# Kernel tuning notes

Measured on AMD Instinct MI355X. Metric: run time of the kernel, lower is better.

Reference implementation:

```python
import jax, jax.numpy as jnp
import numpy as np

CROP_H = 14
CROP_W = 14
EXTRAPOLATION_VALUE = 0.0


def _crop_and_resize(image, boxes, box_ind, crop_h, crop_w, extrapolation_value):
    # image: [B, C, H, W], boxes: [N, 4] normalized (y1, x1, y2, x2), box_ind: [N]
    B, C, H, W = image.shape
    y1, x1, y2, x2 = boxes[:, 0], boxes[:, 1], boxes[:, 2], boxes[:, 3]

    # TF crop_and_resize coordinate mapping (crop_h, crop_w > 1 case)
    height_scale = (y2 - y1) * (H - 1) / (crop_h - 1)  # [N]
    width_scale = (x2 - x1) * (W - 1) / (crop_w - 1)   # [N]
    iy = jnp.arange(crop_h, dtype=image.dtype)
    ix = jnp.arange(crop_w, dtype=image.dtype)
    in_y = y1[:, None] * (H - 1) + iy[None, :] * height_scale[:, None]  # [N, crop_h]
    in_x = x1[:, None] * (W - 1) + ix[None, :] * width_scale[:, None]   # [N, crop_w]

    valid_y = (in_y >= 0) & (in_y <= H - 1)  # [N, crop_h]
    valid_x = (in_x >= 0) & (in_x <= W - 1)  # [N, crop_w]

    top = jnp.floor(in_y)
    left = jnp.floor(in_x)
    ly = (in_y - top)[:, :, None, None]   # [N, crop_h, 1, 1]
    lx = (in_x - left)[:, None, :, None]  # [N, 1, crop_w, 1]

    top_i = jnp.clip(top.astype(jnp.int32), 0, H - 1)          # [N, crop_h]
    bot_i = jnp.clip(top_i + 1, 0, H - 1)
    left_i = jnp.clip(left.astype(jnp.int32), 0, W - 1)        # [N, crop_w]
    right_i = jnp.clip(left_i + 1, 0, W - 1)

    b = box_ind[:, None, None]            # [N, 1, 1]
    yt = top_i[:, :, None]                # [N, crop_h, 1]
    yb = bot_i[:, :, None]
    xl = left_i[:, None, :]               # [N, 1, crop_w]
    xr = right_i[:, None, :]

    # advanced indexing -> [N, crop_h, crop_w, C]
    tl = image[b, :, yt, xl]
    tr = image[b, :, yt, xr]
    bl = image[b, :, yb, xl]
    br = image[b, :, yb, xr]

    top_v = tl + (tr - tl) * lx
    bot_v = bl + (br - bl) * lx
    val = top_v + (bot_v - top_v) * ly    # [N, crop_h, crop_w, C]

    mask = (valid_y[:, :, None] & valid_x[:, None, :])[:, :, :, None]
    val = jnp.where(mask, val, jnp.asarray(extrapolation_value, image.dtype))
    return jnp.transpose(val, (0, 3, 1, 2))  # [N, C, crop_h, crop_w]


def setup_inputs() -> dict:
    key = jax.random.key(0)
    k1, k2, k3 = jax.random.split(key, 3)
    B, C, H, W = 8, 256, 200, 200
    N = 1000
    image = jax.random.normal(k1, (B, C, H, W), dtype=jnp.float32)
    boxes = jax.random.uniform(k2, (N, 4), dtype=jnp.float32)
    box_ind = jax.random.randint(k3, (N,), 0, B, dtype=jnp.int32)
    return {"image": image, "boxes": boxes, "box_ind": box_ind}


def reference(image, boxes, box_ind):
    return _crop_and_resize(image, boxes, box_ind, CROP_H, CROP_W, EXTRAPOLATION_VALUE)
```

## Files before the change

### kernel.cpp

```cpp
#include <hip/hip_runtime.h>


#define CROP_H 14
#define CROP_W 14
#define C_DIM 256
#define H_DIM 200
#define W_DIM 200
#define PER_BOX (C_DIM * CROP_H * CROP_W)
#define BLOCK 256

__global__ __launch_bounds__(BLOCK) void crop_and_resize_kernel(
    const float* __restrict__ image,
    const float* __restrict__ boxes,
    const int*   __restrict__ box_ind,
    float*       __restrict__ out)
{
    __shared__ int   s_ti[CROP_H], s_bi[CROP_H];
    __shared__ int   s_li[CROP_W], s_ri[CROP_W];
    __shared__ float s_ly[CROP_H], s_lx[CROP_W];
    __shared__ int   s_vy[CROP_H], s_vx[CROP_W];
    __shared__ int   s_b;

    const int n = blockIdx.x;
    const int t = threadIdx.x;

    if (t == 0) s_b = box_ind[n];
    if (t < CROP_H + CROP_W) {
        const float y1 = boxes[n * 4 + 0];
        const float x1 = boxes[n * 4 + 1];
        const float y2 = boxes[n * 4 + 2];
        const float x2 = boxes[n * 4 + 3];
        if (t < CROP_H) {
            const int iy = t;
            const float hs   = (y2 - y1) * (float)(H_DIM - 1) / (float)(CROP_H - 1);
            const float in_y = y1 * (float)(H_DIM - 1) + (float)iy * hs;
            const int   vy   = (in_y >= 0.0f) && (in_y <= (float)(H_DIM - 1));
            const float top  = floorf(in_y);
            const float ly   = in_y - top;
            int ti = (int)top;
            ti = min(max(ti, 0), H_DIM - 1);
            const int bi = min(ti + 1, H_DIM - 1);
            s_ti[iy] = ti; s_bi[iy] = bi; s_ly[iy] = ly; s_vy[iy] = vy;
        } else {
            const int ix = t - CROP_H;
            const float ws   = (x2 - x1) * (float)(W_DIM - 1) / (float)(CROP_W - 1);
            const float in_x = x1 * (float)(W_DIM - 1) + (float)ix * ws;
            const int   vx   = (in_x >= 0.0f) && (in_x <= (float)(W_DIM - 1));
            const float left = floorf(in_x);
            const float lx   = in_x - left;
            int li = (int)left;
            li = min(max(li, 0), W_DIM - 1);
            const int ri = min(li + 1, W_DIM - 1);
            s_li[ix] = li; s_ri[ix] = ri; s_lx[ix] = lx; s_vx[ix] = vx;
        }
    }
    __syncthreads();

    const int b = s_b;
    const float* __restrict__ imgb = image + (size_t)b * C_DIM * H_DIM * W_DIM;
    float* __restrict__ outb = out + (size_t)n * PER_BOX;

    for (int j = t; j < PER_BOX; j += BLOCK) {
        const int c  = j / (CROP_H * CROP_W);
        const int p  = j - c * (CROP_H * CROP_W);
        const int iy = p / CROP_W;
        const int ix = p - iy * CROP_W;

        float v = 0.0f;
        if (s_vy[iy] & s_vx[ix]) {
            const float* __restrict__ base = imgb + (size_t)c * (H_DIM * W_DIM);
            const int ti = s_ti[iy], bi = s_bi[iy];
            const int li = s_li[ix], ri = s_ri[ix];
            const float tl = base[ti * W_DIM + li];
            const float tr = base[ti * W_DIM + ri];
            const float bl = base[bi * W_DIM + li];
            const float br = base[bi * W_DIM + ri];
            const float lx = s_lx[ix];
            const float ly = s_ly[iy];
            const float top_v = tl + (tr - tl) * lx;
            const float bot_v = bl + (br - bl) * lx;
            v = top_v + (bot_v - top_v) * ly;
        }
        outb[j] = v;
    }
}

extern "C" void kernel_launch(void* const* d_in, const int* in_sizes, int n_in,
                              void* d_out, int out_size, void* d_ws, size_t ws_size,
                              hipStream_t stream) {
    const float* image   = (const float*)d_in[0];
    const float* boxes   = (const float*)d_in[1];
    const int*   box_ind = (const int*)d_in[2];
    float*       out     = (float*)d_out;

    const int N = in_sizes[2];

    crop_and_resize_kernel<<<dim3(N), dim3(BLOCK), 0, stream>>>(image, boxes, box_ind, out);
}
```

Measured before the change: 778.0 us.

## Sort boxes by batch index and split channels across blocks for cache locality

Adds a single-block counting-sort kernel that orders boxes by batch image, so consecutive blocks read the same image and share L2/MALL cache. Each box is split into four channel chunks across blocks for more parallelism. Loads are now unconditional with a select at the end, and the inner loop is unrolled. The cost is an extra kernel launch and a serial one-block sort, plus wasted loads for invalid sample points.

```diff
diff --git a/kernel.cpp b/kernel.cpp
--- a/kernel.cpp
+++ b/kernel.cpp
@@ -6,13 +6,39 @@
 #define C_DIM 256
 #define H_DIM 200
 #define W_DIM 200
+#define HW (H_DIM * W_DIM)
 #define PER_BOX (C_DIM * CROP_H * CROP_W)
 #define BLOCK 256
+#define CHUNKS 4
+#define C_PER (C_DIM / CHUNKS)
+#define ELEMS (C_PER * CROP_H * CROP_W)
+
+__global__ __launch_bounds__(BLOCK) void sort_boxes_kernel(
+    const int* __restrict__ box_ind, int N, int* __restrict__ perm)
+{
+    __shared__ int cnt[8];
+    __shared__ int base[8];
+    const int t = threadIdx.x;
+    if (t < 8) cnt[t] = 0;
+    __syncthreads();
+    for (int i = t; i < N; i += BLOCK) atomicAdd(&cnt[box_ind[i]], 1);
+    __syncthreads();
+    if (t == 0) {
+        int run = 0;
+        for (int b = 0; b < 8; ++b) { base[b] = run; run += cnt[b]; }
+    }
+    __syncthreads();
+    for (int i = t; i < N; i += BLOCK) {
+        const int pos = atomicAdd(&base[box_ind[i]], 1);
+        perm[pos] = i;
+    }
+}
 
 __global__ __launch_bounds__(BLOCK) void crop_and_resize_kernel(
     const float* __restrict__ image,
     const float* __restrict__ boxes,
     const int*   __restrict__ box_ind,
+    const int*   __restrict__ perm,
     float*       __restrict__ out)
 {
     __shared__ int   s_ti[CROP_H], s_bi[CROP_H];
@@ -21,8 +47,14 @@
     __shared__ int   s_vy[CROP_H], s_vx[CROP_W];
     __shared__ int   s_b;
 
-    const int n = blockIdx.x;
-    const int t = threadIdx.x;
+    const int slot  = blockIdx.x / CHUNKS;
+    const int chunk = blockIdx.x % CHUNKS;
+    const int t     = threadIdx.x;
+
+    __shared__ int s_n;
+    if (t == 0) s_n = perm[slot];
+    __syncthreads();
+    const int n = s_n;
 
     if (t == 0) s_b = box_ind[n];
     if (t < CROP_H + CROP_W) {
@@ -56,31 +88,33 @@
     }
     __syncthreads();
 
-    const int b = s_b;
-    const float* __restrict__ imgb = image + (size_t)b * C_DIM * H_DIM * W_DIM;
-    float* __restrict__ outb = out + (size_t)n * PER_BOX;
+    const float* __restrict__ imgb = image + (size_t)s_b * (C_DIM * HW)
+                                           + (size_t)chunk * (C_PER * HW);
+    float* __restrict__ outb = out + (size_t)n * PER_BOX + (size_t)chunk * ELEMS;
 
-    for (int j = t; j < PER_BOX; j += BLOCK) {
+    #pragma unroll 4
+    for (int j = t; j < ELEMS; j += BLOCK) {
         const int c  = j / (CROP_H * CROP_W);
         const int p  = j - c * (CROP_H * CROP_W);
         const int iy = p / CROP_W;
         const int ix = p - iy * CROP_W;
 
-        float v = 0.0f;
-        if (s_vy[iy] & s_vx[ix]) {
-            const float* __restrict__ base = imgb + (size_t)c * (H_DIM * W_DIM);
-            const int ti = s_ti[iy], bi = s_bi[iy];
-            const int li = s_li[ix], ri = s_ri[ix];
-            const float tl = base[ti * W_DIM + li];
-            const float tr = base[ti * W_DIM + ri];
-            const float bl = base[bi * W_DIM + li];
-            const float br = base[bi * W_DIM + ri];
-            const float lx = s_lx[ix];
-            const float ly = s_ly[iy];
-            const float top_v = tl + (tr - tl) * lx;
-            const float bot_v = bl + (br - bl) * lx;
-            v = top_v + (bot_v - top_v) * ly;
-        }
+        const int ti = s_ti[iy], bi = s_bi[iy];
+        const int li = s_li[ix], ri = s_ri[ix];
+        const float* __restrict__ base = imgb + (size_t)c * HW;
+
+        const float tl = base[ti * W_DIM + li];
+        const float tr = base[ti * W_DIM + ri];
+        const float bl = base[bi * W_DIM + li];
+        const float br = base[bi * W_DIM + ri];
+
+        const float lx = s_lx[ix];
+        const float ly = s_ly[iy];
+        const float top_v = tl + (tr - tl) * lx;
+        const float bot_v = bl + (br - bl) * lx;
+        float v = top_v + (bot_v - top_v) * ly;
+
+        v = (s_vy[iy] & s_vx[ix]) ? v : 0.0f;
         outb[j] = v;
     }
 }
@@ -92,8 +126,11 @@
     const float* boxes   = (const float*)d_in[1];
     const int*   box_ind = (const int*)d_in[2];
     float*       out     = (float*)d_out;
+    int*         perm    = (int*)d_ws;
 
     const int N = in_sizes[2];
 
-    crop_and_resize_kernel<<<dim3(N), dim3(BLOCK), 0, stream>>>(image, boxes, box_ind, out);
+    sort_boxes_kernel<<<dim3(1), dim3(BLOCK), 0, stream>>>(box_ind, N, perm);
+    crop_and_resize_kernel<<<dim3(N * CHUNKS), dim3(BLOCK), 0, stream>>>(
+        image, boxes, box_ind, perm, out);
 }
```

New measurement: 704.6 us. 9.4% less time.
